# Optimization experiments

Hardware: AMD Instinct MI355X
Metric: run time of the kernel (lower is better)

## Reference

```python
import jax, jax.numpy as jnp
import numpy as np

STRIDES = (8, 16, 32)
FEAT_SIZES = ((80, 80), (40, 40), (20, 20))  # (h, w) per level for 640x640 input
OFFSET = 0.5
NMS_K = 300
IOU_THR = 0.65
EPS = 1e-7


def make_priors():
    """MlvlPointGenerator.grid_priors with with_stride=True, flattened over levels."""
    pts, strs = [], []
    for (h, w), s in zip(FEAT_SIZES, STRIDES):
        xs = (jnp.arange(w, dtype=jnp.float32) + OFFSET) * s
        ys = (jnp.arange(h, dtype=jnp.float32) + OFFSET) * s
        yy, xx = jnp.meshgrid(ys, xs, indexing='ij')
        pts.append(jnp.stack([xx.reshape(-1), yy.reshape(-1)], -1))
        strs.append(jnp.full((h * w, 2), float(s), dtype=jnp.float32))
    return jnp.concatenate(pts, 0), jnp.concatenate(strs, 0)  # [N,2], [N,2]


def pairwise_iou(boxes):  # boxes [K,4] xyxy
    area = jnp.clip(boxes[:, 2] - boxes[:, 0], 0) * jnp.clip(boxes[:, 3] - boxes[:, 1], 0)
    lt = jnp.maximum(boxes[:, None, :2], boxes[None, :, :2])
    rb = jnp.minimum(boxes[:, None, 2:], boxes[None, :, 2:])
    wh = jnp.clip(rb - lt, 0)
    inter = wh[..., 0] * wh[..., 1]
    union = area[:, None] + area[None, :] - inter
    return inter / (union + EPS)


def nms_keep(boxes):  # boxes [K,4] sorted by descending score -> bool keep mask [K]
    K = boxes.shape[0]
    iou = pairwise_iou(boxes)
    idx = jnp.arange(K)

    def body(i, keep):
        sup = (iou[i] > IOU_THR) & (idx > i) & keep[i]
        return keep & ~sup

    return jax.lax.fori_loop(0, K, body, jnp.ones((K,), dtype=bool))


def setup_inputs() -> dict:
    key = jax.random.key(0)
    k1, k2, k3, k4, k5 = jax.random.split(key, 5)
    B, N, K = 128, 8400, 17
    return {
        'cls_scores': jax.random.normal(k1, (B, N, 1), jnp.float32),
        'bbox_preds': jax.random.normal(k2, (B, N, 4), jnp.float32),
        'objectness': jax.random.normal(k3, (B, N), jnp.float32),
        'kpt_offsets': jax.random.normal(k4, (B, N, K, 2), jnp.float32),
        'kpt_vis_preds': jax.random.normal(k5, (B, N, K), jnp.float32),
    }


def reference(cls_scores, bbox_preds, objectness, kpt_offsets, kpt_vis_preds):
    priors, strides = make_priors()  # [N,2] each
    # bbox decode: center-offset + exp wh, YOLOX style
    xy = bbox_preds[..., :2] * strides + priors            # [B,N,2]
    wh = jnp.exp(bbox_preds[..., 2:4]) * strides           # [B,N,2]
    boxes = jnp.concatenate([xy - wh * 0.5, xy + wh * 0.5], -1)  # [B,N,4]
    scores = jax.nn.sigmoid(cls_scores[..., 0]) * jax.nn.sigmoid(objectness)  # [B,N]
    # keypoint decode
    kpts = kpt_offsets * strides[:, None, :] + priors[:, None, :]  # [B,N,K,2]
    B, N, K, _ = kpts.shape
    kpts_flat = kpts.reshape(B, N, K * 2)
    vis = jax.nn.sigmoid(kpt_vis_preds)                    # [B,N,K]
    # fixed-size top-k pre-NMS selection
    top_vals, top_idx = jax.lax.top_k(scores, NMS_K)       # [B,NMS_K]
    gather = lambda x: jnp.take_along_axis(x, top_idx[..., None], axis=1)
    boxes_k = gather(boxes)       # [B,NMS_K,4]
    kpts_k = gather(kpts_flat)    # [B,NMS_K,2K]
    vis_k = gather(vis)           # [B,NMS_K,K]
    keep = jax.vmap(nms_keep)(boxes_k)                      # [B,NMS_K] bool
    final_scores = top_vals * keep.astype(top_vals.dtype)
    # [B, NMS_K, 4 + 1 + 2K + K]
    return jnp.concatenate([boxes_k, final_scores[..., None], kpts_k, vis_k], -1)
```

## Files before the change

kernel.cpp:

```cpp
#include <hip/hip_runtime.h>
#include <math.h>

#define BATCH 128
#define NANCH 8400
#define NMSK  300
#define KPT   17
#define OUTC  56
#define CAND  1024
#define NTHR  1024
#define NBIN  8192
#define BSHIFT 19
#define NGRP  (NANCH / 4)
#define HPAD(i) ((i) + ((i) >> 3))
#define HSZ   (NBIN + NBIN / 8)

__device__ __forceinline__ void prior_of(int i, float& stride, float& cx, float& cy) {
    int row, col;
    if (i < 6400)      { stride = 8.0f;  row = i / 80;              col = i - row * 80; }
    else if (i < 8000) { int ii = i - 6400; stride = 16.0f; row = ii / 40; col = ii - row * 40; }
    else               { int ii = i - 8000; stride = 32.0f; row = ii / 20; col = ii - row * 20; }
    cx = ((float)col + 0.5f) * stride;
    cy = ((float)row + 0.5f) * stride;
}

__global__ __launch_bounds__(NTHR, 4) void fused_kernel(
    const float* __restrict__ cls, const float* __restrict__ obj,
    const float* __restrict__ bbox, const float* __restrict__ kofs,
    const float* __restrict__ kvis, float* __restrict__ out)
{
    const int b    = blockIdx.x;
    const int tid  = threadIdx.x;
    const int lane = tid & 63;
    const int wv   = tid >> 6;

    __shared__ __align__(16) unsigned int hist[HSZ];
    __shared__ unsigned int wtot[16], wab[16];
    __shared__ unsigned int sh_pivot, sh_cnt;
    __shared__ unsigned long long ckey[CAND];
    __shared__ float bx1[NMSK], by1[NMSK], bx2[NMSK], by2[NMSK], area[NMSK];
    __shared__ float sval[NMSK];
    __shared__ int   sidx[NMSK];
    __shared__ unsigned long long supl[NMSK * 6];
    __shared__ unsigned long long keepw[5];

    unsigned int sck[12];
    {
        const float4* c4 = (const float4*)(cls + (size_t)b * NANCH);
        const float4* o4 = (const float4*)(obj + (size_t)b * NANCH);
        #pragma unroll
        for (int k = 0; k < 3; ++k) {
            int g = tid + k * NTHR;
            if (g < NGRP) {
                float4 cv = c4[g];
                float4 ov = o4[g];
                float sa0 = 1.0f / (1.0f + (float)exp(-(double)cv.x));
                float sa1 = 1.0f / (1.0f + (float)exp(-(double)cv.y));
                float sa2 = 1.0f / (1.0f + (float)exp(-(double)cv.z));
                float sa3 = 1.0f / (1.0f + (float)exp(-(double)cv.w));
                float so0 = 1.0f / (1.0f + (float)exp(-(double)ov.x));
                float so1 = 1.0f / (1.0f + (float)exp(-(double)ov.y));
                float so2 = 1.0f / (1.0f + (float)exp(-(double)ov.z));
                float so3 = 1.0f / (1.0f + (float)exp(-(double)ov.w));
                sck[4 * k + 0] = __float_as_uint(sa0 * so0);
                sck[4 * k + 1] = __float_as_uint(sa1 * so1);
                sck[4 * k + 2] = __float_as_uint(sa2 * so2);
                sck[4 * k + 3] = __float_as_uint(sa3 * so3);
            } else {
                sck[4 * k + 0] = 0u; sck[4 * k + 1] = 0u;
                sck[4 * k + 2] = 0u; sck[4 * k + 3] = 0u;
            }
        }
        #pragma unroll
        for (int k = 0; k < 9; ++k) {
            int i = tid + k * NTHR;
            if (i < HSZ) hist[i] = 0u;
        }
        if (tid == 0) sh_cnt = 0u;
    }
    __syncthreads();

    #pragma unroll
    for (int k = 0; k < 3; ++k) {
        int g = tid + k * NTHR;
        if (g < NGRP) {
            atomicAdd(&hist[HPAD(sck[4 * k + 0] >> BSHIFT)], 1u);
            atomicAdd(&hist[HPAD(sck[4 * k + 1] >> BSHIFT)], 1u);
            atomicAdd(&hist[HPAD(sck[4 * k + 2] >> BSHIFT)], 1u);
            atomicAdd(&hist[HPAD(sck[4 * k + 3] >> BSHIFT)], 1u);
        }
    }
    __syncthreads();

    unsigned int s7[8];
    {
        unsigned int hh[8];
        #pragma unroll
        for (int k = 0; k < 8; ++k) hh[k] = hist[9 * tid + k];
        s7[7] = hh[7];
        s7[6] = s7[7] + hh[6]; s7[5] = s7[6] + hh[5]; s7[4] = s7[5] + hh[4];
        s7[3] = s7[4] + hh[3]; s7[2] = s7[3] + hh[2]; s7[1] = s7[2] + hh[1];
        s7[0] = s7[1] + hh[0];
    }
    unsigned int T = s7[0];
    unsigned int v = T;
    #pragma unroll
    for (int d = 1; d < 64; d <<= 1) {
        unsigned int t2 = (unsigned int)__shfl_down((int)v, d, 64);
        if (lane + d < 64) v += t2;
    }
    unsigned int aiw = v - T;
    if (lane == 0) wtot[wv] = v;
    __syncthreads();
    if (tid < 16) {
        unsigned int wa = 0;
        for (int q = tid + 1; q < 16; ++q) wa += wtot[q];
        wab[tid] = wa;
    }
    __syncthreads();

    {
        unsigned int ag = wab[wv] + aiw;
        #pragma unroll
        for (int k = 0; k < 8; ++k) {
            unsigned int ge = ag + s7[k];
            unsigned int gn = (k < 7) ? (ag + s7[k + 1]) : ag;
            if (ge >= NMSK && gn < NMSK) sh_pivot = 8u * (unsigned)tid + (unsigned)k;
        }
    }
    __syncthreads();
    unsigned int pivot_bits = sh_pivot << BSHIFT;

    #pragma unroll
    for (int k = 0; k < 3; ++k) {
        int g = tid + k * NTHR;
        bool valid = (g < NGRP);
        #pragma unroll
        for (int s = 0; s < 4; ++s) {
            unsigned int key = sck[4 * k + s];
            bool pred = valid && (key >= pivot_bits);
            unsigned long long m = __ballot(pred);
            unsigned int cnt = (unsigned int)__popcll(m);
            unsigned int wbase = 0u;
            if (lane == 0 && cnt) wbase = atomicAdd(&sh_cnt, cnt);
            wbase = (unsigned int)__shfl((int)wbase, 0, 64);
            if (pred) {
                unsigned int p = wbase + (unsigned int)__popcll(m & ((1ull << lane) - 1ull));
                unsigned int idx = 4u * (unsigned)g + (unsigned)s;
                if (p < CAND)
                    ckey[p] = ((unsigned long long)key << 32)
                            | (unsigned long long)(0xFFFFFFFFu - idx);
            }
        }
    }
    __syncthreads();
    unsigned int M = sh_cnt; if (M > CAND) M = CAND;

    if (tid < (int)M) {
        unsigned long long mine = ckey[tid];
        int rank = 0;
        for (unsigned int t2 = 0; t2 < M; ++t2) rank += (ckey[t2] > mine) ? 1 : 0;
        if (rank < NMSK) {
            int i = (int)(0xFFFFFFFFu - (unsigned int)(mine & 0xFFFFFFFFull));
            sidx[rank] = i;
            sval[rank] = __uint_as_float((unsigned int)(mine >> 32));
            float stride, cx, cy;
            prior_of(i, stride, cx, cy);
            float4 bb = *(const float4*)(bbox + ((size_t)b * NANCH + (size_t)i) * 4);
            float x = bb.x * stride + cx;
            float y = bb.y * stride + cy;
            float w = expf(bb.z) * stride;
            float h = expf(bb.w) * stride;
            float x1 = x - 0.5f * w, y1 = y - 0.5f * h;
            float x2 = x + 0.5f * w, y2 = y + 0.5f * h;
            bx1[rank] = x1; by1[rank] = y1; bx2[rank] = x2; by2[rank] = y2;
            area[rank] = fmaxf(x2 - x1, 0.0f) * fmaxf(y2 - y1, 0.0f);
        }
    }
    __syncthreads();

    for (int t = tid; t < NMSK * 5; t += NTHR) {
        int w = t / NMSK;
        int i = t - w * NMSK;
        int jlo = w * 64; if (jlo < i + 1) jlo = i + 1;
        int jhi = w * 64 + 64; if (jhi > NMSK) jhi = NMSK;
        unsigned long long m = 0;
        float ax1 = bx1[i], ay1 = by1[i], ax2 = bx2[i], ay2 = by2[i], aa = area[i];
        for (int j = jlo; j < jhi; ++j) {
            float lx = fmaxf(ax1, bx1[j]);
            float ly = fmaxf(ay1, by1[j]);
            float rx = fminf(ax2, bx2[j]);
            float ry = fminf(ay2, by2[j]);
            float iw = fmaxf(rx - lx, 0.0f);
            float ih = fmaxf(ry - ly, 0.0f);
            float inter = iw * ih;
            float iou = inter / (aa + area[j] - inter + 1e-7f);
            if (iou > 0.65f) m |= 1ull << (j & 63);
        }
        supl[i * 6 + w] = m;
    }
    __syncthreads();

    if (tid < 64) {
        int j = tid;
        unsigned long long keep0 = ~0ull, keep1 = ~0ull, keep2 = ~0ull, keep3 = ~0ull;
        unsigned long long keep4 = (1ull << (NMSK - 256)) - 1ull;
        #define CHUNK(C, KC, IMAX) { \
            int r = (C) * 64 + j; \
            unsigned int lo0=0,hi0=0,lo1=0,hi1=0,lo2=0,hi2=0,lo3=0,hi3=0,lo4=0,hi4=0; \
            if (r < NMSK) { \
                unsigned long long w0 = supl[r*6+0], w1 = supl[r*6+1], w2 = supl[r*6+2]; \
                unsigned long long w3 = supl[r*6+3], w4 = supl[r*6+4]; \
                lo0=(unsigned int)w0; hi0=(unsigned int)(w0>>32); \
                lo1=(unsigned int)w1; hi1=(unsigned int)(w1>>32); \
                lo2=(unsigned int)w2; hi2=(unsigned int)(w2>>32); \
                lo3=(unsigned int)w3; hi3=(unsigned int)(w3>>32); \
                lo4=(unsigned int)w4; hi4=(unsigned int)(w4>>32); } \
            _Pragma("clang loop unroll(disable)") \
            for (int bi = 0; bi < (IMAX); ++bi) { \
                if ((KC >> bi) & 1ull) { \
                    unsigned long long s0 = ((unsigned long long)__builtin_amdgcn_readlane(hi0,bi)<<32) | __builtin_amdgcn_readlane(lo0,bi); \
                    unsigned long long s1 = ((unsigned long long)__builtin_amdgcn_readlane(hi1,bi)<<32) | __builtin_amdgcn_readlane(lo1,bi); \
                    unsigned long long s2 = ((unsigned long long)__builtin_amdgcn_readlane(hi2,bi)<<32) | __builtin_amdgcn_readlane(lo2,bi); \
                    unsigned long long s3 = ((unsigned long long)__builtin_amdgcn_readlane(hi3,bi)<<32) | __builtin_amdgcn_readlane(lo3,bi); \
                    unsigned long long s4 = ((unsigned long long)__builtin_amdgcn_readlane(hi4,bi)<<32) | __builtin_amdgcn_readlane(lo4,bi); \
                    keep0 &= ~s0; keep1 &= ~s1; keep2 &= ~s2; keep3 &= ~s3; keep4 &= ~s4; } } }
        CHUNK(0, keep0, 64)
        CHUNK(1, keep1, 64)
        CHUNK(2, keep2, 64)
        CHUNK(3, keep3, 64)
        CHUNK(4, keep4, NMSK - 256)
        #undef CHUNK
        if (j == 0) { keepw[0]=keep0; keepw[1]=keep1; keepw[2]=keep2; keepw[3]=keep3; keepw[4]=keep4; }
    } else {
        const float* kof = kofs + (size_t)b * NANCH * 34;
        const float* kvi = kvis + (size_t)b * NANCH * KPT;
        float* ob = out + (size_t)b * NMSK * OUTC;
        for (int t = tid - 64; t < NMSK * 4; t += NTHR - 64) {
            int j = t >> 2, ci = t & 3;
            float vv = (ci == 0) ? bx1[j] : (ci == 1) ? by1[j] : (ci == 2) ? bx2[j] : by2[j];
            ob[j * OUTC + ci] = vv;
        }
        for (int e = tid - 64; e < NMSK * 51; e += NTHR - 64) {
            int j  = e / 51;
            int ci = e - j * 51;
            int i  = sidx[j];
            float vv;
            if (ci < 34) {
                float stride, cx, cy;
                prior_of(i, stride, cx, cy);
                float off = kof[(size_t)i * 34 + ci];
                vv = off * stride + ((ci & 1) ? cy : cx);
            } else {
                float x = kvi[(size_t)i * KPT + (ci - 34)];
                vv = 1.0f / (1.0f + expf(-x));
            }
            ob[j * OUTC + 5 + ci] = vv;
        }
    }
    __syncthreads();

    if (tid < NMSK) {
        bool kp = (keepw[tid >> 6] >> (tid & 63)) & 1ull;
        out[(size_t)b * NMSK * OUTC + (size_t)tid * OUTC + 4] = kp ? sval[tid] : 0.0f;
    }
}

extern "C" void kernel_launch(void* const* d_in, const int* in_sizes, int n_in,
                              void* d_out, int out_size, void* d_ws, size_t ws_size,
                              hipStream_t stream) {
    const float* cls  = (const float*)d_in[0];
    const float* bbox = (const float*)d_in[1];
    const float* obj  = (const float*)d_in[2];
    const float* kofs = (const float*)d_in[3];
    const float* kvis = (const float*)d_in[4];
    float* out = (float*)d_out;

    (void)d_ws; (void)ws_size;

    fused_kernel<<<BATCH, NTHR, 0, stream>>>(cls, obj, bbox, kofs, kvis, out);
}
```

Baseline: 297.9 us.

## Split fused kernel into score/top-k head and NMS/gather tail kernels

Splits the single fused per-batch kernel into two launches. The head kernel does scoring, top-k selection and box decode, then writes the candidate table to a global workspace. The tail kernel reloads that table and runs NMS and the output gather. The intent is to reduce the shared memory and register footprint of each kernel, at the cost of an extra launch and a global round trip.

Measured after the change: 299.7 us. No clear change (+0.6%).

```diff
diff --git a/kernel.cpp b/kernel.cpp
--- a/kernel.cpp
+++ b/kernel.cpp
@@ -13,6 +13,7 @@
 #define NGRP  (NANCH / 4)
 #define HPAD(i) ((i) + ((i) >> 3))
 #define HSZ   (NBIN + NBIN / 8)
+#define WSTRIDE 2112
 
 __device__ __forceinline__ void prior_of(int i, float& stride, float& cx, float& cy) {
     int row, col;
@@ -23,10 +24,9 @@
     cy = ((float)row + 0.5f) * stride;
 }
 
-__global__ __launch_bounds__(NTHR, 4) void fused_kernel(
+__global__ __launch_bounds__(NTHR, 4) void head_kernel(
     const float* __restrict__ cls, const float* __restrict__ obj,
-    const float* __restrict__ bbox, const float* __restrict__ kofs,
-    const float* __restrict__ kvis, float* __restrict__ out)
+    const float* __restrict__ bbox, unsigned int* __restrict__ ws)
 {
     const int b    = blockIdx.x;
     const int tid  = threadIdx.x;
@@ -40,8 +40,6 @@
     __shared__ float bx1[NMSK], by1[NMSK], bx2[NMSK], by2[NMSK], area[NMSK];
     __shared__ float sval[NMSK];
     __shared__ int   sidx[NMSK];
-    __shared__ unsigned long long supl[NMSK * 6];
-    __shared__ unsigned long long keepw[5];
 
     unsigned int sck[12];
     {
@@ -174,6 +172,52 @@
             float x2 = x + 0.5f * w, y2 = y + 0.5f * h;
             bx1[rank] = x1; by1[rank] = y1; bx2[rank] = x2; by2[rank] = y2;
             area[rank] = fmaxf(x2 - x1, 0.0f) * fmaxf(y2 - y1, 0.0f);
+        }
+    }
+    __syncthreads();
+
+    for (int t = tid; t < 7 * NMSK; t += NTHR) {
+        int r = t / NMSK;
+        int j = t - r * NMSK;
+        unsigned int w;
+        switch (r) {
+            case 0:  w = (unsigned int)sidx[j];      break;
+            case 1:  w = __float_as_uint(sval[j]);   break;
+            case 2:  w = __float_as_uint(bx1[j]);    break;
+            case 3:  w = __float_as_uint(by1[j]);    break;
+            case 4:  w = __float_as_uint(bx2[j]);    break;
+            case 5:  w = __float_as_uint(by2[j]);    break;
+            default: w = __float_as_uint(area[j]);   break;
+        }
+        ws[(size_t)b * WSTRIDE + t] = w;
+    }
+}
+
+__global__ __launch_bounds__(NTHR, 4) void tail_kernel(
+    const unsigned int* __restrict__ ws, const float* __restrict__ kofs,
+    const float* __restrict__ kvis, float* __restrict__ out)
+{
+    const int b   = blockIdx.x;
+    const int tid = threadIdx.x;
+
+    __shared__ float bx1[NMSK], by1[NMSK], bx2[NMSK], by2[NMSK], area[NMSK];
+    __shared__ float sval[NMSK];
+    __shared__ int   sidx[NMSK];
+    __shared__ unsigned long long supl[NMSK * 6];
+    __shared__ unsigned long long keepw[5];
+
+    for (int t = tid; t < 7 * NMSK; t += NTHR) {
+        unsigned int w = ws[(size_t)b * WSTRIDE + t];
+        int r = t / NMSK;
+        int j = t - r * NMSK;
+        switch (r) {
+            case 0:  sidx[j] = (int)w;               break;
+            case 1:  sval[j] = __uint_as_float(w);   break;
+            case 2:  bx1[j]  = __uint_as_float(w);   break;
+            case 3:  by1[j]  = __uint_as_float(w);   break;
+            case 4:  bx2[j]  = __uint_as_float(w);   break;
+            case 5:  by2[j]  = __uint_as_float(w);   break;
+            default: area[j] = __uint_as_float(w);   break;
         }
     }
     __syncthreads();
@@ -275,7 +319,8 @@
     const float* kvis = (const float*)d_in[4];
     float* out = (float*)d_out;
 
-    (void)d_ws; (void)ws_size;
-
-    fused_kernel<<<BATCH, NTHR, 0, stream>>>(cls, obj, bbox, kofs, kvis, out);
+    unsigned int* ws = (unsigned int*)d_ws;
+
+    head_kernel<<<BATCH, NTHR, 0, stream>>>(cls, obj, bbox, ws);
+    tail_kernel<<<BATCH, NTHR, 0, stream>>>(ws, kofs, kvis, out);
 }
```
